# Kernel tuning notes

Measured on AMD Instinct MI355X. Metric: run time of the kernel, lower is better.

The kernel has to match this reference:

```python
import jax, jax.numpy as jnp
from jax import lax
import numpy as np

B = 32          # batch
E = 768         # embedding_dim == hidden_dim (required for the module to run)
V = 8192        # vocabulary_size
MAX_LEN = 256   # max_seq_length


def setup_inputs() -> dict:
    key = jax.random.key(0)
    ks = jax.random.split(key, 10)
    s = 0.02
    return {
        "latent": jax.random.normal(ks[0], (B, E), jnp.float32),
        "W_lat": jax.random.normal(ks[1], (E, E), jnp.float32) * s,
        "b_lat": jnp.zeros((E,), jnp.float32),
        "emb":   jax.random.normal(ks[2], (V, E), jnp.float32) * s,
        "W_ih":  jax.random.normal(ks[3], (3 * E, E), jnp.float32) * s,
        "W_hh":  jax.random.normal(ks[4], (3 * E, E), jnp.float32) * s,
        "b_ih":  jnp.zeros((3 * E,), jnp.float32),
        "b_hh":  jnp.zeros((3 * E,), jnp.float32),
        "W_out": jax.random.normal(ks[5], (V, E), jnp.float32) * s,
        "b_out": jnp.zeros((V,), jnp.float32),
    }


def reference(latent, W_lat, b_lat, emb, W_ih, W_hh, b_ih, b_hh, W_out, b_out):
    # initial hidden state: projected latent, shape [B, E]
    h0 = latent @ W_lat.T + b_lat
    # decoder starts from token id 1 (<sos>)
    tok0 = jnp.ones((latent.shape[0],), jnp.int32)

    def step(carry, _):
        h, tok = carry
        x = emb[tok]                                  # [B, E] embedding lookup
        gi = x @ W_ih.T + b_ih                        # [B, 3E]
        gh = h @ W_hh.T + b_hh                        # [B, 3E]
        i_r, i_z, i_n = jnp.split(gi, 3, axis=-1)
        h_r, h_z, h_n = jnp.split(gh, 3, axis=-1)
        r = jax.nn.sigmoid(i_r + h_r)
        z = jax.nn.sigmoid(i_z + h_z)
        n = jnp.tanh(i_n + r * h_n)
        h_new = (1.0 - z) * n + z * h                 # torch GRU cell update
        pred = h_new @ W_out.T + b_out                # [B, V]
        tok_new = jnp.argmax(pred, axis=-1).astype(jnp.int32)  # greedy decode
        return (h_new, tok_new), pred

    _, preds = lax.scan(step, (h0, tok0), None, length=MAX_LEN)  # [T, B, V]
    return preds.transpose(1, 0, 2)                               # [B, T, V]
```

## Files before the change

### kernel.cpp

```cpp
#include <hip/hip_runtime.h>
#include <stdint.h>


typedef unsigned long long u64;
typedef unsigned int u32;
typedef _Float16 f16;
using half8 = __attribute__((ext_vector_type(8))) _Float16;
using f32x4 = __attribute__((ext_vector_type(4))) float;
using uint4v = __attribute__((ext_vector_type(4))) unsigned int;

#define E_ 768
#define V_ 8192
#define T_ 256
#define HP 24576
#define IH_PLANE (2304*768)
#define OUT_PLANE (8192*768)
#define NBLK 256

#define AGENT_LD(p)    __hip_atomic_load((p), __ATOMIC_RELAXED, __HIP_MEMORY_SCOPE_AGENT)
#define AGENT_ST(p,v)  __hip_atomic_store((p), (v), __ATOMIC_RELAXED, __HIP_MEMORY_SCOPE_AGENT)
#define AGENT_ADD(p,v) __hip_atomic_fetch_add((p), (v), __ATOMIC_RELAXED, __HIP_MEMORY_SCOPE_AGENT)

__device__ __forceinline__ f32x4 mfma16(half8 a, half8 b, f32x4 c){
  return __builtin_amdgcn_mfma_f32_16x16x32_f16(a, b, c, 0, 0, 0);
}
__device__ __forceinline__ void split2(float f, f16& hi, f16& lo){
  f16 h = (f16)f; hi = h; lo = (f16)((f - (float)h) * 4096.0f);
}
__device__ __forceinline__ u32 packh(float f){
  f16 h, l; split2(f, h, l);
  return (u32)__builtin_bit_cast(unsigned short, h) |
         ((u32)__builtin_bit_cast(unsigned short, l) << 16);
}
__device__ __forceinline__ float unpackh(u32 u){
  f16 h = __builtin_bit_cast(f16, (unsigned short)(u & 0xffffu));
  f16 l = __builtin_bit_cast(f16, (unsigned short)(u >> 16));
  return (float)h + (float)l * (1.0f/4096.0f);
}
__device__ __forceinline__ u64 packkey(float f, int v){
  u32 fb = __float_as_uint(f);
  u32 s  = fb ^ ((u32)((int32_t)fb>>31) | 0x80000000u);
  return ((u64)s<<32) | (u64)(0xFFFFFFFFu - (u32)v);
}

#define NB_CONV 1200
#define NB_H0   96
#define NG_IH   221184
#define NG_ALL  1228800

__global__ __launch_bounds__(256) void prep_k(
    const float* __restrict__ W_ih, const float* __restrict__ W_hh, const float* __restrict__ W_out,
    const float* __restrict__ latent, const float* __restrict__ W_lat, const float* __restrict__ b_lat,
    f16* __restrict__ Wih_s, f16* __restrict__ Whh_s, f16* __restrict__ Wout_s,
    float* __restrict__ h_f32, u32* __restrict__ h_seq, unsigned* __restrict__ bar)
{
  int blk = blockIdx.x;
  if (blk < NB_CONV){
    for (int g = blk*256 + threadIdx.x; g < NG_ALL; g += NB_CONV*256){
      const float* src; f16* hi; f16* lo; int off;
      if (g < NG_IH)        { src=W_ih; hi=Wih_s; lo=Wih_s+IH_PLANE; off=g*8; }
      else if (g < 2*NG_IH) { src=W_hh; hi=Whh_s; lo=Whh_s+IH_PLANE; off=(g-NG_IH)*8; }
      else                  { src=W_out; hi=Wout_s; lo=Wout_s+OUT_PLANE; off=(g-2*NG_IH)*8; }
      float4 a = *(const float4*)(src+off);
      float4 b = *(const float4*)(src+off+4);
      float fs[8] = {a.x,a.y,a.z,a.w,b.x,b.y,b.z,b.w};
      half8 vh, vl;
      #pragma unroll
      for (int j=0;j<8;j++){ f16 h,l; split2(fs[j],h,l); vh[j]=h; vl[j]=l; }
      *(half8*)(hi+off) = vh;
      *(half8*)(lo+off) = vl;
    }
  } else {
    if (blk==NB_CONV) bar[threadIdx.x] = 0;
    int tid = (blk-NB_CONV)*256 + threadIdx.x;
    int b = tid/768, e = tid - b*768;
    const float4* wr = (const float4*)(W_lat + (size_t)e*768);
    const float4* xr = (const float4*)(latent + (size_t)b*768);
    float s0=0.f,s1=0.f,s2=0.f,s3=0.f;
    for (int k=0;k<192;k++){
      float4 w = wr[k]; float4 x = xr[k];
      s0 += w.x*x.x; s1 += w.y*x.y; s2 += w.z*x.z; s3 += w.w*x.w;
    }
    float acc = b_lat[e] + ((s0+s1)+(s2+s3));
    h_f32[b*768+e] = acc;
    h_seq[b*768+e] = packh(acc);
  }
}

__global__ __launch_bounds__(512) void gitab_k(
    const float* __restrict__ emb, const f16* __restrict__ Wih_s, u32* __restrict__ gi_tab)
{
  __shared__ float red[3][8][2][64][4];
  const int bid = blockIdx.x, tid = threadIdx.x;
  const int tb = bid>>1, half = bid&1;
  const int w = tid>>6, lane = tid&63, col = lane&15, kg = lane>>4, kc = w;
  half8 ah[2][3], al[2][3];
  #pragma unroll
  for (int m=0;m<2;m++)
    #pragma unroll
    for (int i=0;i<3;i++){
      const float* src = emb + (size_t)(tb*32 + m*16 + col)*768 + kc*96 + i*32 + kg*8;
      float4 x0 = *(const float4*)src, x1 = *(const float4*)(src+4);
      float fs[8] = {x0.x,x0.y,x0.z,x0.w,x1.x,x1.y,x1.z,x1.w};
      half8 vh, vl;
      #pragma unroll
      for (int j=0;j<8;j++){ f16 h,l; split2(fs[j],h,l); vh[j]=h; vl[j]=l; }
      ah[m][i]=vh; al[m][i]=vl;
    }
  for (int g=0; g<24; ++g){
    #pragma unroll
    for (int j=0;j<3;j++){
      const int nt = half*72 + g*3 + j;
      f32x4 a0[2], a1[2];
      #pragma unroll
      for (int m=0;m<2;m++){ a0[m]=f32x4{0,0,0,0}; a1[m]=f32x4{0,0,0,0}; }
      #pragma unroll
      for (int i=0;i<3;i++){
        size_t o = (size_t)(nt*16+col)*768 + kc*96 + i*32 + kg*8;
        half8 bh = *(const half8*)(Wih_s + o);
        half8 bl = *(const half8*)(Wih_s + IH_PLANE + o);
        #pragma unroll
        for (int m=0;m<2;m++){
          a0[m] = mfma16(ah[m][i], bh, a0[m]);
          a1[m] = mfma16(ah[m][i], bl, a1[m]);
          a1[m] = mfma16(al[m][i], bh, a1[m]);
        }
      }
      #pragma unroll
      for (int m=0;m<2;m++){
        f32x4 v;
        #pragma unroll
        for (int r=0;r<4;r++) v[r] = a0[m][r] + a1[m][r]*(1.0f/4096.0f);
        *(f32x4*)&red[j][w][m][lane][0] = v;
      }
    }
    __syncthreads();
    if (w < 6){
      const int j = w>>1, m = w&1;
      f32x4 s = {0,0,0,0};
      #pragma unroll
      for (int ww=0; ww<8; ww++) s += *(const f32x4*)&red[j][ww][m][lane][0];
      const int nt = half*72 + g*3 + j;
      const int tokr = tb*32 + m*16 + kg*4;
      #pragma unroll
      for (int r=0;r<4;r++)
        gi_tab[(size_t)(tokr+r)*2304 + nt*16 + col] = packh(s[r]);
    }
    __syncthreads();
  }
}

__device__ __forceinline__ void gridbar(unsigned* bar, unsigned target){
  __syncthreads();
  if (threadIdx.x == 0){
    const int g = blockIdx.x & 7;
    unsigned old = AGENT_ADD(&bar[g*16], 1u);
    if (old == 32u*target - 1u)
      AGENT_ADD(&bar[128], 1u);
    int spins = 0;
    while (AGENT_LD(&bar[128]) < 8u*target){
      __builtin_amdgcn_s_sleep(1);
      if ((++spins & 2047) == 0)
        AGENT_ADD(&bar[128], 0u);
    }
  }
  __syncthreads();
}

__global__ __launch_bounds__(512, 2) void decode_k(
    const f16* __restrict__ Wout_s, const f16* __restrict__ Whh_s, const u32* __restrict__ gi_tab,
    float* __restrict__ gh_buf, const float* __restrict__ h_f32, u32* __restrict__ h_seq,
    u64* __restrict__ candbufT, const float* __restrict__ b_ih, const float* __restrict__ b_hh,
    const float* __restrict__ b_out, float* __restrict__ out, unsigned* __restrict__ bar)
{
  __shared__ float red[3][8][2][64][4];
  __shared__ u64 amkey[32];
  const int bid = blockIdx.x, tid = threadIdx.x;
  const int w = tid>>6, lane = tid&63, col = lane&15, kg = lane>>4, kc = w;

  __builtin_amdgcn_fence(__ATOMIC_ACQUIRE, "agent");
  __syncthreads();

  const f16* srcH[3] = {Wout_s, Wout_s, (bid<144)? Whh_s : Wout_s};
  const f16* srcL[3] = {Wout_s+OUT_PLANE, Wout_s+OUT_PLANE,
                        (bid<144)? Whh_s+IH_PLANE : Wout_s+OUT_PLANE};
  const int  rowb[3] = {bid*16, 4096+bid*16, (bid<144)? bid*16 : 0};
  half8 bf_h[3][3], bf_l[3][3];
  #pragma unroll
  for (int s=0;s<3;s++)
    #pragma unroll
    for (int i=0;i<3;i++){
      size_t o = (size_t)(rowb[s]+col)*768 + kc*96 + i*32 + kg*8;
      bf_h[s][i] = *(const half8*)(srcH[s] + o);
      bf_l[s][i] = *(const half8*)(srcL[s] + o);
    }
  float bo_reg[2];
  bo_reg[0] = b_out[bid*16 + col];
  bo_reg[1] = b_out[4096 + bid*16 + col];

  int cb = 0, ce = 0; float hreg = 0.f;
  float bir=0,biz=0,bin_=0,bhr=0,bhz=0,bhn=0;
  if (bid < 48){
    int gid = bid*512 + tid;
    cb = gid/768; ce = gid - cb*768;
    hreg = h_f32[cb*768 + ce];
    bir=b_ih[ce]; biz=b_ih[768+ce]; bin_=b_ih[1536+ce];
    bhr=b_hh[ce]; bhz=b_hh[768+ce]; bhn=b_hh[1536+ce];
  }

  unsigned bt = 0;
  for (int t=0; t<=256; ++t){
    if (tid < 32) amkey[tid] = 0;
    const u32* hbase = h_seq + (size_t)t*HP;
    uint4v qa[2][3], qb[2][3];
    #pragma unroll
    for (int m=0;m<2;m++)
      #pragma unroll
      for (int i=0;i<3;i++){
        const uint4v* hp = (const uint4v*)(hbase + (m*16+col)*768 + kc*96 + i*32 + kg*8);
        qa[m][i] = hp[0];
        qb[m][i] = hp[1];
      }
    half8 ah[2][3], al[2][3];
    #pragma unroll
    for (int m=0;m<2;m++)
      #pragma unroll
      for (int i=0;i<3;i++){
        uint4v wh, wl;
        u32 d[8] = {qa[m][i][0],qa[m][i][1],qa[m][i][2],qa[m][i][3],
                    qb[m][i][0],qb[m][i][1],qb[m][i][2],qb[m][i][3]};
        #pragma unroll
        for (int j=0;j<4;j++){
          u32 w0 = d[2*j], w1 = d[2*j+1];
          wh[j] = (w0 & 0xffffu) | (w1 << 16);
          wl[j] = (w0 >> 16) | (w1 & 0xffff0000u);
        }
        ah[m][i] = __builtin_bit_cast(half8, wh);
        al[m][i] = __builtin_bit_cast(half8, wl);
      }
    #pragma unroll
    for (int s=0;s<3;s++){
      f32x4 a0[2], a1[2];
      #pragma unroll
      for (int m=0;m<2;m++){ a0[m]=f32x4{0,0,0,0}; a1[m]=f32x4{0,0,0,0}; }
      #pragma unroll
      for (int i=0;i<3;i++)
        #pragma unroll
        for (int m=0;m<2;m++){
          a0[m] = mfma16(ah[m][i], bf_h[s][i], a0[m]);
          a1[m] = mfma16(ah[m][i], bf_l[s][i], a1[m]);
          a1[m] = mfma16(al[m][i], bf_h[s][i], a1[m]);
        }
      #pragma unroll
      for (int m=0;m<2;m++){
        f32x4 v;
        #pragma unroll
        for (int r=0;r<4;r++) v[r] = a0[m][r] + a1[m][r]*(1.0f/4096.0f);
        *(f32x4*)&red[s][w][m][lane][0] = v;
      }
    }
    __syncthreads();
    float sv[2][4];
    bool have_out = false;
    if (w < 3){
      const int s = w;
      float vm[2][4];
      #pragma unroll
      for (int m=0;m<2;m++){
        f32x4 sum = {0,0,0,0};
        #pragma unroll
        for (int ww=0; ww<8; ww++) sum += *(const f32x4*)&red[s][ww][m][lane][0];
        #pragma unroll
        for (int r=0;r<4;r++) vm[m][r] = sum[r];
      }
      if (s < 2){
        if (t >= 1){
          have_out = true;
          const int v = s*4096 + bid*16 + col;
          const float bo = bo_reg[s];
          #pragma unroll
          for (int m=0;m<2;m++)
            #pragma unroll
            for (int r=0;r<4;r++){
              const int b = m*16 + kg*4 + r;
              const float p = vm[m][r] + bo;
              sv[m][r] = p;
              u64 key = packkey(p, v);
              #pragma unroll
              for (int off=1; off<16; off<<=1){
                u64 o = __shfl_xor((unsigned long long)key, off);
                if (o > key) key = o;
              }
              if (col == 0) atomicMax(&amkey[b], key);
            }
        }
      } else if (bid < 144){
        const int gr = bid*16 + col;
        #pragma unroll
        for (int m=0;m<2;m++)
          #pragma unroll
          for (int r=0;r<4;r++)
            AGENT_ST(&gh_buf[(m*16+kg*4+r)*2304 + gr], vm[m][r]);
      }
    }
    __syncthreads();
    if (t >= 1 && tid < 32) AGENT_ST(&candbufT[(size_t)tid*256 + bid], amkey[tid]);
    if (t == 256){
      if (have_out){
        const int v = w*4096 + bid*16 + col;
        #pragma unroll
        for (int m=0;m<2;m++)
          #pragma unroll
          for (int r=0;r<4;r++)
            out[(size_t)(m*16+kg*4+r)*((size_t)T_*V_) + (size_t)(t-1)*V_ + v] = sv[m][r];
      }
      break;
    }
    gridbar(bar, ++bt);
    if (bid >= 48){
      if (have_out){
        const int v = w*4096 + bid*16 + col;
        #pragma unroll
        for (int m=0;m<2;m++)
          #pragma unroll
          for (int r=0;r<4;r++)
            out[(size_t)(m*16+kg*4+r)*((size_t)T_*V_) + (size_t)(t-1)*V_ + v] = sv[m][r];
      }
    } else {
      float* hb = gh_buf + cb*2304 + ce;
      const float ghr0 = AGENT_LD(hb);
      const float ghz0 = AGENT_LD(hb + 768);
      const float ghn0 = AGENT_LD(hb + 1536);
      int tok = 1;
      if (t > 0){
        u64 k = 0;
        #pragma unroll
        for (int j=0;j<4;j++){
          u64 c = AGENT_LD(&candbufT[(size_t)cb*256 + lane + 64*j]);
          if (c > k) k = c;
        }
        #pragma unroll
        for (int off=1; off<64; off<<=1){
          u64 o = __shfl_xor((unsigned long long)k, off);
          if (o > k) k = o;
        }
        tok = (int)(0xFFFFFFFFu - (unsigned)(k & 0xFFFFFFFFull));
      }
      const u32* gp = gi_tab + (size_t)tok*2304 + ce;
      const float gir = unpackh(gp[0])    + bir;
      const float giz = unpackh(gp[768])  + biz;
      const float gin = unpackh(gp[1536]) + bin_;
      const float ghr = ghr0 + bhr;
      const float ghz = ghz0 + bhz;
      const float ghn = ghn0 + bhn;
      const float rr = 1.0f/(1.0f+expf(-(gir+ghr)));
      const float zz = 1.0f/(1.0f+expf(-(giz+ghz)));
      const float nn = tanhf(gin + rr*ghn);
      hreg = (1.0f-zz)*nn + zz*hreg;
      AGENT_ST(&h_seq[(size_t)(t+1)*HP + cb*768 + ce], packh(hreg));
      if (have_out){
        const int v = w*4096 + bid*16 + col;
        #pragma unroll
        for (int m=0;m<2;m++)
          #pragma unroll
          for (int r=0;r<4;r++)
            out[(size_t)(m*16+kg*4+r)*((size_t)T_*V_) + (size_t)(t-1)*V_ + v] = sv[m][r];
      }
    }
    gridbar(bar, ++bt);
  }
}

extern "C" void kernel_launch(void* const* d_in, const int* in_sizes, int n_in,
                              void* d_out, int out_size, void* d_ws, size_t ws_size,
                              hipStream_t stream){
  const float* latent = (const float*)d_in[0];
  const float* W_lat  = (const float*)d_in[1];
  const float* b_lat  = (const float*)d_in[2];
  const float* emb    = (const float*)d_in[3];
  const float* W_ih   = (const float*)d_in[4];
  const float* W_hh   = (const float*)d_in[5];
  const float* b_ih   = (const float*)d_in[6];
  const float* b_hh   = (const float*)d_in[7];
  const float* W_out  = (const float*)d_in[8];
  const float* b_out  = (const float*)d_in[9];
  float* out = (float*)d_out;
  (void)in_sizes; (void)n_in; (void)out_size; (void)ws_size;

  char* ws = (char*)d_ws;
  size_t off = 0;
  auto carve = [&](size_t bytes)->char*{
    char* p = ws + off; off += (bytes + 255) & ~(size_t)255; return p;
  };
  f16*      Wih_s  = (f16*)     carve((size_t)2*IH_PLANE*2);
  f16*      Whh_s  = (f16*)     carve((size_t)2*IH_PLANE*2);
  f16*      Wout_s = (f16*)     carve((size_t)2*OUT_PLANE*2);
  u32*      gi_tab = (u32*)     carve((size_t)8192*2304*4);
  float*    gh_buf = (float*)   carve((size_t)32*2304*4);
  float*    h_f32  = (float*)   carve((size_t)HP*4);
  u32*      h_seq  = (u32*)     carve((size_t)257*HP*4);
  u64*      candbufT=(u64*)     carve((size_t)32*256*8);
  unsigned* bar    = (unsigned*)carve(2048);

  hipLaunchKernelGGL(prep_k, dim3(NB_CONV+NB_H0), dim3(256), 0, stream,
                     W_ih, W_hh, W_out, latent, W_lat, b_lat,
                     Wih_s, Whh_s, Wout_s, h_f32, h_seq, bar);
  hipLaunchKernelGGL(gitab_k, dim3(512), dim3(512), 0, stream, emb, Wih_s, gi_tab);

  void* kargs[] = {
    (void*)&Wout_s, (void*)&Whh_s, (void*)&gi_tab, (void*)&gh_buf, (void*)&h_f32,
    (void*)&h_seq, (void*)&candbufT, (void*)&b_ih, (void*)&b_hh, (void*)&b_out,
    (void*)&out, (void*)&bar
  };
  (void)hipLaunchCooperativeKernel((void*)decode_k, dim3(NBLK), dim3(512), kargs, 0, stream);
}
```

Measured before the change: 3.120 ms.

## Split grid barrier into arrive/wait with separate hidden-state barrier for GRU blocks

Replaces the two full grid barriers per step with a split scheme. All blocks arrive on the first barrier, but only the 48 GRU-update blocks wait on it. Those blocks then signal a second, smaller counter once the new hidden state is written, and every block waits only on that counter. Output-writing blocks therefore no longer spin on the first barrier, so their logits stores can overlap the GRU update, at the cost of more complex counter bookkeeping and a second counter region to zero.

```diff
diff --git a/kernel.cpp b/kernel.cpp
--- a/kernel.cpp
+++ b/kernel.cpp
@@ -71,7 +71,7 @@
       *(half8*)(lo+off) = vl;
     }
   } else {
-    if (blk==NB_CONV) bar[threadIdx.x] = 0;
+    if (blk==NB_CONV){ bar[threadIdx.x] = 0; bar[256+threadIdx.x] = 0; }
     int tid = (blk-NB_CONV)*256 + threadIdx.x;
     int b = tid/768, e = tid - b*768;
     const float4* wr = (const float4*)(W_lat + (size_t)e*768);
@@ -150,21 +150,12 @@
   }
 }
 
-__device__ __forceinline__ void gridbar(unsigned* bar, unsigned target){
-  __syncthreads();
-  if (threadIdx.x == 0){
-    const int g = blockIdx.x & 7;
-    unsigned old = AGENT_ADD(&bar[g*16], 1u);
-    if (old == 32u*target - 1u)
-      AGENT_ADD(&bar[128], 1u);
-    int spins = 0;
-    while (AGENT_LD(&bar[128]) < 8u*target){
-      __builtin_amdgcn_s_sleep(1);
-      if ((++spins & 2047) == 0)
-        AGENT_ADD(&bar[128], 0u);
-    }
+__device__ __forceinline__ void pollroot(unsigned* p, u32 goal){
+  int spins = 0;
+  while (AGENT_LD(p) < goal){
+    __builtin_amdgcn_s_sleep(1);
+    if ((++spins & 2047) == 0) AGENT_ADD(p, 0u);
   }
-  __syncthreads();
 }
 
 __global__ __launch_bounds__(512, 2) void decode_k(
@@ -208,7 +199,6 @@
     bhr=b_hh[ce]; bhz=b_hh[768+ce]; bhn=b_hh[1536+ce];
   }
 
-  unsigned bt = 0;
   for (int t=0; t<=256; ++t){
     if (tid < 32) amkey[tid] = 0;
     const u32* hbase = h_seq + (size_t)t*HP;
@@ -316,17 +306,15 @@
       }
       break;
     }
-    gridbar(bar, ++bt);
-    if (bid >= 48){
-      if (have_out){
-        const int v = w*4096 + bid*16 + col;
-        #pragma unroll
-        for (int m=0;m<2;m++)
-          #pragma unroll
-          for (int r=0;r<4;r++)
-            out[(size_t)(m*16+kg*4+r)*((size_t)T_*V_) + (size_t)(t-1)*V_ + v] = sv[m][r];
-      }
-    } else {
+    const u32 stp = (u32)(t+1);
+    __syncthreads();
+    if (tid == 0){
+      unsigned old = AGENT_ADD(&bar[(bid&7)*16], 1u);
+      if (old == 32u*stp - 1u) AGENT_ADD(&bar[128], 1u);
+    }
+    if (bid < 48){
+      if (tid == 0) pollroot(&bar[128], 8u*stp);
+      __syncthreads();
       float* hb = gh_buf + cb*2304 + ce;
       const float ghr0 = AGENT_LD(hb);
       const float ghz0 = AGENT_LD(hb + 768);
@@ -358,6 +346,11 @@
       const float nn = tanhf(gin + rr*ghn);
       hreg = (1.0f-zz)*nn + zz*hreg;
       AGENT_ST(&h_seq[(size_t)(t+1)*HP + cb*768 + ce], packh(hreg));
+      __syncthreads();
+      if (tid == 0){
+        unsigned old = AGENT_ADD(&bar[192 + (bid&7)*16], 1u);
+        if (old == 6u*stp - 1u) AGENT_ADD(&bar[320], 1u);
+      }
       if (have_out){
         const int v = w*4096 + bid*16 + col;
         #pragma unroll
@@ -366,8 +359,18 @@
           for (int r=0;r<4;r++)
             out[(size_t)(m*16+kg*4+r)*((size_t)T_*V_) + (size_t)(t-1)*V_ + v] = sv[m][r];
       }
-    }
-    gridbar(bar, ++bt);
+    } else {
+      if (have_out){
+        const int v = w*4096 + bid*16 + col;
+        #pragma unroll
+        for (int m=0;m<2;m++)
+          #pragma unroll
+          for (int r=0;r<4;r++)
+            out[(size_t)(m*16+kg*4+r)*((size_t)T_*V_) + (size_t)(t-1)*V_ + v] = sv[m][r];
+      }
+    }
+    if (tid == 0) pollroot(&bar[320], 8u*stp);
+    __syncthreads();
   }
 }
 
```

Result: no change. 3.114 ms (-0.2%).
